# Performance work log

Hardware: AMD Instinct MI355X
Metric: run time of the kernel (lower is better)

The kernel has to match this reference:

```python
import jax, jax.numpy as jnp
import numpy as np

NEG_SLOPE = 0.01  # nn.LeakyReLU default


def gcn_conv(x, src, dst, deg_inv_sqrt, W, b, n_nodes):
    """PyG GCNConv with self-loops already folded into (src, dst, deg_inv_sqrt).
    out = scatter_add(norm_e * (x @ W)[src]) + b, norm_e = d_src^-1/2 * d_dst^-1/2."""
    h = x @ W  # [N, F_out] -- transform first (F_out < F_in saves gather traffic)
    norm = (deg_inv_sqrt[src] * deg_inv_sqrt[dst])[:, None]  # [E, 1]
    msg = h[src] * norm  # [E, F_out]
    return jax.ops.segment_sum(msg, dst, num_segments=n_nodes) + b


def setup_inputs() -> dict:
    key = jax.random.key(0)
    ks = jax.random.split(key, 8)
    N, E, F_IN, F_HID, F_OUT = 50000, 800000, 256, 128, 64
    x = jax.random.normal(ks[0], (N, F_IN), dtype=jnp.float32)
    edge_index = jax.random.randint(ks[1], (2, E), 0, N, dtype=jnp.int64)
    def glorot(k, shape):
        lim = float(np.sqrt(6.0 / (shape[0] + shape[1])))
        return jax.random.uniform(k, shape, jnp.float32, -lim, lim)
    return {
        "x": x,
        "edge_index": edge_index,
        "W1": glorot(ks[2], (F_IN, F_HID)),
        "b1": jnp.zeros((F_HID,), jnp.float32),
        "W_mu": glorot(ks[3], (F_HID, F_OUT)),
        "b_mu": jnp.zeros((F_OUT,), jnp.float32),
        "W_logvar": glorot(ks[4], (F_HID, F_OUT)),
        "b_logvar": jnp.zeros((F_OUT,), jnp.float32),
    }


def reference(x, edge_index, W1, b1, W_mu, b_mu, W_logvar, b_logvar):
    n_nodes = x.shape[0]
    loops = jnp.arange(n_nodes, dtype=edge_index.dtype)
    src = jnp.concatenate([edge_index[0], loops])
    dst = jnp.concatenate([edge_index[1], loops])
    # degree on destination nodes (includes self-loop); >= 1 so rsqrt is safe
    deg = jax.ops.segment_sum(jnp.ones_like(dst, dtype=x.dtype), dst, num_segments=n_nodes)
    deg_inv_sqrt = jax.lax.rsqrt(deg)

    h = gcn_conv(x, src, dst, deg_inv_sqrt, W1, b1, n_nodes)
    h = jax.nn.leaky_relu(h, NEG_SLOPE)
    mu = gcn_conv(h, src, dst, deg_inv_sqrt, W_mu, b_mu, n_nodes)
    logvar = gcn_conv(h, src, dst, deg_inv_sqrt, W_logvar, b_logvar, n_nodes)
    return (mu, logvar)
```

## Files before the change

### kernel.cpp

```cpp
#include <hip/hip_runtime.h>

#define NEG_SLOPE 0.01f
#define EPB 4096
#define NB_SHIFT 8

typedef __attribute__((ext_vector_type(8))) short bf16x8;
typedef __attribute__((ext_vector_type(4))) float floatx4;

__device__ __forceinline__ short f2bf(float f) {
    union { float f; unsigned u; } v; v.f = f;
    unsigned u = v.u;
    u += 0x7FFF + ((u >> 16) & 1);
    return (short)(u >> 16);
}
__device__ __forceinline__ float bf2f(short s) {
    union { unsigned u; float f; } v;
    v.u = ((unsigned)(unsigned short)s) << 16;
    return v.f;
}


__launch_bounds__(256)
__global__ void hist_pack(const int* __restrict__ dst, int E, int B, int K,
                          int* __restrict__ btot,
                          const float* __restrict__ W1, const float* __restrict__ Wmu,
                          const float* __restrict__ Wlv,
                          short* __restrict__ w1f, short* __restrict__ wcatf) {
    __shared__ int lh[256];
    int bid = blockIdx.x;
    if (bid < B) {
        lh[threadIdx.x] = 0;
        __syncthreads();
        int lo = bid * EPB, hi = min(lo + EPB, E);
        for (int e = lo + threadIdx.x; e < hi; e += 256)
            atomicAdd(&lh[dst[e] >> NB_SHIFT], 1);
        __syncthreads();
        int v = lh[threadIdx.x];
        if (v) atomicAdd(&btot[threadIdx.x], v);
    } else {
        int i = (bid - B) * 256 + threadIdx.x;
        if (i < 128 * 256) {
            int j  = i & 7;
            int ln = (i >> 3) & 15;
            int q  = (i >> 7) & 3;
            int t  = (i >> 9) & 7;
            int kb = i >> 12;
            int n = t * 16 + ln;
            int k = kb * 32 + q * 8 + j;
            w1f[i] = f2bf(W1[k * 128 + n]);
        } else {
            int i2 = i - 128 * 256;
            int j  = i2 & 7;
            int ln = (i2 >> 3) & 15;
            int q  = (i2 >> 7) & 3;
            int t  = (i2 >> 9) & 7;
            int kb = i2 >> 12;
            int n = t * 16 + ln;
            int k = kb * 32 + q * 8 + j;
            wcatf[i2] = f2bf((n < 64) ? Wmu[k * 64 + n] : Wlv[k * 64 + (n - 64)]);
        }
    }
}

__global__ void bucket_scan(const int* __restrict__ btot, int K, int E,
                            int* __restrict__ bstart, int* __restrict__ bcur) {
    __shared__ int waveTot[4];
    __shared__ int waveOff[4];
    int tid = threadIdx.x;
    int lane = tid & 63, wave = tid >> 6;
    int v = (tid < K) ? btot[tid] : 0;
    int s = v;
    #pragma unroll
    for (int o = 1; o < 64; o <<= 1) {
        int t = __shfl_up(s, o);
        if (lane >= o) s += t;
    }
    if (lane == 63) waveTot[wave] = s;
    __syncthreads();
    if (tid == 0) {
        int acc = 0;
        #pragma unroll
        for (int w = 0; w < 4; w++) { waveOff[w] = acc; acc += waveTot[w]; }
    }
    __syncthreads();
    int excl = s - v + waveOff[wave];
    if (tid < K) { bstart[tid] = excl; bcur[tid] = excl; }
    if (tid == 0) bstart[K] = E;
}


template<int K, bool ABF16, bool SCALE>
__device__ __forceinline__ void gemm_body(int blk, int tid, const void* __restrict__ Ap,
                                          const short* __restrict__ Bfrag,
                                          short* __restrict__ C, int M,
                                          const float* __restrict__ dis) {
    int w = tid >> 6;
    int lane = tid & 63;
    int ln = lane & 15;
    int q  = lane >> 4;
    int rowTile = blk * 128 + w * 32;

    int r0 = rowTile + ln;
    int r1 = rowTile + 16 + ln;
    int r0c = (r0 < M) ? r0 : (M - 1);
    int r1c = (r1 < M) ? r1 : (M - 1);

    const float* a0F = (const float*)Ap + (size_t)r0c * K + q * 8;
    const float* a1F = (const float*)Ap + (size_t)r1c * K + q * 8;
    const short* a0B = (const short*)Ap + (size_t)r0c * K + q * 8;
    const short* a1B = (const short*)Ap + (size_t)r1c * K + q * 8;
    const short* bLane = Bfrag + lane * 8;

    floatx4 acc[2][8];
    #pragma unroll
    for (int f = 0; f < 2; f++)
        #pragma unroll
        for (int t = 0; t < 8; t++) acc[f][t] = (floatx4){0.f, 0.f, 0.f, 0.f};

    constexpr int NIT = K / 32;
    #pragma unroll
    for (int kb = 0; kb < NIT; kb++) {
        int kt = kb * 32;
        bf16x8 aF0, aF1;
        if (ABF16) {
            aF0 = *(const bf16x8*)(a0B + kt);
            aF1 = *(const bf16x8*)(a1B + kt);
        } else {
            float4 x0 = *(const float4*)(a0F + kt);
            float4 x1 = *(const float4*)(a0F + kt + 4);
            float4 y0 = *(const float4*)(a1F + kt);
            float4 y1 = *(const float4*)(a1F + kt + 4);
            aF0[0] = f2bf(x0.x); aF0[1] = f2bf(x0.y); aF0[2] = f2bf(x0.z); aF0[3] = f2bf(x0.w);
            aF0[4] = f2bf(x1.x); aF0[5] = f2bf(x1.y); aF0[6] = f2bf(x1.z); aF0[7] = f2bf(x1.w);
            aF1[0] = f2bf(y0.x); aF1[1] = f2bf(y0.y); aF1[2] = f2bf(y0.z); aF1[3] = f2bf(y0.w);
            aF1[4] = f2bf(y1.x); aF1[5] = f2bf(y1.y); aF1[6] = f2bf(y1.z); aF1[7] = f2bf(y1.w);
        }
        bf16x8 bF[8];
        #pragma unroll
        for (int t = 0; t < 8; t++)
            bF[t] = *(const bf16x8*)(bLane + (size_t)(kb * 8 + t) * 512);
        #pragma unroll
        for (int t = 0; t < 8; t++) {
            acc[0][t] = __builtin_amdgcn_mfma_f32_16x16x32_bf16(aF0, bF[t], acc[0][t], 0, 0, 0);
            acc[1][t] = __builtin_amdgcn_mfma_f32_16x16x32_bf16(aF1, bF[t], acc[1][t], 0, 0, 0);
        }
    }

    #pragma unroll
    for (int f = 0; f < 2; f++) {
        #pragma unroll
        for (int reg = 0; reg < 4; reg++) {
            int r = rowTile + f * 16 + q * 4 + reg;
            if (r < M) {
                float s = SCALE ? dis[r] : 1.f;
                #pragma unroll
                for (int t = 0; t < 8; t++)
                    C[(size_t)r * 128 + t * 16 + ln] = f2bf(s * acc[f][t][reg]);
            }
        }
    }
}

__launch_bounds__(256)
__global__ void scatter_gemm1(const int* __restrict__ src, const int* __restrict__ dst,
                              int E, int B, int* __restrict__ bcur,
                              unsigned* __restrict__ bucketed,
                              const float* __restrict__ x, const short* __restrict__ w1f,
                              short* __restrict__ z1, int M) {
    __shared__ int lh[256];
    __shared__ int lofs[256];
    __shared__ int gbase[256];
    __shared__ unsigned srt[EPB];
    __shared__ int waveTot[4];
    __shared__ int waveOff[4];
    int bid = blockIdx.x;
    int tid = threadIdx.x;
    if (bid < B) {
        lh[tid] = 0;
        __syncthreads();
        int lo = bid * EPB, hi = min(lo + EPB, E);
        for (int e = lo + tid; e < hi; e += 256)
            atomicAdd(&lh[dst[e] >> NB_SHIFT], 1);
        __syncthreads();
        int v = lh[tid];
        int lane = tid & 63, wave = tid >> 6;
        int s = v;
        #pragma unroll
        for (int o = 1; o < 64; o <<= 1) {
            int t = __shfl_up(s, o);
            if (lane >= o) s += t;
        }
        if (lane == 63) waveTot[wave] = s;
        __syncthreads();
        if (tid == 0) {
            int acc = 0;
            #pragma unroll
            for (int w = 0; w < 4; w++) { waveOff[w] = acc; acc += waveTot[w]; }
        }
        __syncthreads();
        int excl = s - v + waveOff[wave];
        lofs[tid] = excl;
        if (v) gbase[tid] = atomicAdd(&bcur[tid], v);
        __syncthreads();
        lh[tid] = excl;
        __syncthreads();
        for (int e = lo + tid; e < hi; e += 256) {
            int d = dst[e];
            unsigned rec = (unsigned)(src[e] & 0xFFFF) | ((unsigned)d << 16);
            int p = atomicAdd(&lh[d >> NB_SHIFT], 1);
            srt[p] = rec;
        }
        __syncthreads();
        int cnt = hi - lo;
        for (int p = tid; p < cnt; p += 256) {
            unsigned r = srt[p];
            int k = r >> 24;
            bucketed[gbase[k] + (p - lofs[k])] = r;
        }
    } else {
        gemm_body<256, false, false>(bid - B, tid, (const void*)x, w1f, z1, M, nullptr);
    }
}

__global__ void fill_csr_deg(const unsigned* __restrict__ bucketed,
                             const int* __restrict__ bstart,
                             int* __restrict__ row_ptr, int* __restrict__ row_end,
                             float* __restrict__ dis,
                             unsigned short* __restrict__ csr_src, int N) {
    __shared__ int cnt[256];
    __shared__ int rp[256];
    __shared__ int waveTot[4];
    __shared__ int waveOff[4];
    __shared__ unsigned short lcsr[8192];
    int k = blockIdx.x;
    int tid = threadIdx.x;
    int base = k << NB_SHIFT;
    cnt[tid] = 0;
    __syncthreads();
    int lo = bstart[k], hi = bstart[k + 1];
    int m = hi - lo;
    for (int e = lo + tid; e < hi; e += 256)
        atomicAdd(&cnt[(bucketed[e] >> 16) & 255], 1);
    __syncthreads();
    int v = cnt[tid];
    int lane = tid & 63, wave = tid >> 6;
    int s = v;
    #pragma unroll
    for (int o = 1; o < 64; o <<= 1) {
        int t = __shfl_up(s, o);
        if (lane >= o) s += t;
    }
    if (lane == 63) waveTot[wave] = s;
    __syncthreads();
    if (tid == 0) {
        int acc = 0;
        #pragma unroll
        for (int w = 0; w < 4; w++) { waveOff[w] = acc; acc += waveTot[w]; }
    }
    __syncthreads();
    int excl = s - v + waveOff[wave];
    rp[tid] = excl;
    int node = base + tid;
    if (node < N) {
        row_ptr[node] = lo + excl;
        row_end[node] = lo + excl + v;
        dis[node] = rsqrtf(1.0f + (float)v);
    }
    __syncthreads();
    if (m <= 8192) {
        for (int e = lo + tid; e < hi; e += 256) {
            unsigned sd = bucketed[e];
            int p = atomicAdd(&rp[(sd >> 16) & 255], 1);
            lcsr[p] = (unsigned short)(sd & 0xFFFFu);
        }
        __syncthreads();
        for (int i = tid; i < m; i += 256) csr_src[lo + i] = lcsr[i];
    } else {
        for (int e = lo + tid; e < hi; e += 256) {
            unsigned sd = bucketed[e];
            int p = atomicAdd(&rp[(sd >> 16) & 255], 1);
            csr_src[lo + p] = (unsigned short)(sd & 0xFFFFu);
        }
    }
}


__launch_bounds__(256)
__global__ void agg_layer1(const short* __restrict__ z1, const int* __restrict__ row_ptr,
                           const int* __restrict__ row_end,
                           const unsigned short* __restrict__ csr_src,
                           const float* __restrict__ dis, const float* __restrict__ b1,
                           short* __restrict__ h, int N) {
    int wave = threadIdx.x >> 6;
    int node = blockIdx.x * 4 + wave;
    if (node >= N) return;
    int lane = threadIdx.x & 63;
    int qi = lane >> 4;
    int fl = lane & 15;
    int fo = fl * 8;
    const short* zb = z1 + fo;
    int start = row_ptr[node], end = row_end[node];
    float acc[8];
    #pragma unroll
    for (int t = 0; t < 8; t++) acc[t] = 0.f;
    for (int bse = start; bse < end; bse += 64) {
        int n = end - bse; n = (n > 64) ? 64 : n;
        int idx = (int)csr_src[bse + ((lane < n) ? lane : 0)];
        float dl = dis[idx];
        for (int j = 0; j < n; j += 8) {
            int j0 = j + qi;
            int j1 = j0 + 4;
            int c0 = (j0 < n) ? j0 : 0;
            int c1 = (j1 < n) ? j1 : 0;
            int s0 = __shfl(idx, c0);
            int s1 = __shfl(idx, c1);
            float d0 = __shfl(dl, c0);
            float d1 = __shfl(dl, c1);
            if (j0 >= n) d0 = 0.f;
            if (j1 >= n) d1 = 0.f;
            bf16x8 z0 = *(const bf16x8*)(zb + (size_t)s0 * 128);
            bf16x8 zv1 = *(const bf16x8*)(zb + (size_t)s1 * 128);
            #pragma unroll
            for (int t = 0; t < 8; t++)
                acc[t] = fmaf(d0, bf2f(z0[t]), fmaf(d1, bf2f(zv1[t]), acc[t]));
        }
    }
    if (qi == 0) {
        float dn = dis[node];
        bf16x8 zs = *(const bf16x8*)(zb + (size_t)node * 128);
        #pragma unroll
        for (int t = 0; t < 8; t++) acc[t] = fmaf(dn, bf2f(zs[t]), acc[t]);
    }
    #pragma unroll
    for (int t = 0; t < 8; t++) {
        acc[t] += __shfl_xor(acc[t], 16);
        acc[t] += __shfl_xor(acc[t], 32);
    }
    if (qi == 0) {
        float d = dis[node];
        bf16x8 ov;
        #pragma unroll
        for (int t = 0; t < 8; t++) {
            float v = fmaf(d, acc[t], b1[fo + t]);
            v = (v > 0.f) ? v : NEG_SLOPE * v;
            ov[t] = f2bf(v);
        }
        *(bf16x8*)(h + (size_t)node * 128 + fo) = ov;
    }
}


__launch_bounds__(256)
__global__ void agg_layer2(const short* __restrict__ zp, const int* __restrict__ row_ptr,
                           const int* __restrict__ row_end,
                           const unsigned short* __restrict__ csr_src,
                           const float* __restrict__ dis, const float* __restrict__ b_mu,
                           const float* __restrict__ b_lv, float* __restrict__ out, int N) {
    int wave = threadIdx.x >> 6;
    int node = blockIdx.x * 4 + wave;
    if (node >= N) return;
    int lane = threadIdx.x & 63;
    int qi = lane >> 4;
    int fl = lane & 15;
    int fo = fl * 8;
    const short* zb = zp + fo;
    int start = row_ptr[node], end = row_end[node];
    float acc[8];
    #pragma unroll
    for (int t = 0; t < 8; t++) acc[t] = 0.f;
    for (int bse = start; bse < end; bse += 64) {
        int n = end - bse; n = (n > 64) ? 64 : n;
        int idx = (int)csr_src[bse + ((lane < n) ? lane : 0)];
        for (int j = 0; j < n; j += 8) {
            int j0 = j + qi;
            int j1 = j0 + 4;
            int c0 = (j0 < n) ? j0 : 0;
            int c1 = (j1 < n) ? j1 : 0;
            int s0 = __shfl(idx, c0);
            int s1 = __shfl(idx, c1);
            float w0 = (j0 < n) ? 1.f : 0.f;
            float w1 = (j1 < n) ? 1.f : 0.f;
            bf16x8 z0 = *(const bf16x8*)(zb + (size_t)s0 * 128);
            bf16x8 zv1 = *(const bf16x8*)(zb + (size_t)s1 * 128);
            #pragma unroll
            for (int t = 0; t < 8; t++)
                acc[t] = fmaf(w0, bf2f(z0[t]), fmaf(w1, bf2f(zv1[t]), acc[t]));
        }
    }
    if (qi == 0) {
        bf16x8 zs = *(const bf16x8*)(zb + (size_t)node * 128);
        #pragma unroll
        for (int t = 0; t < 8; t++) acc[t] += bf2f(zs[t]);
    }
    #pragma unroll
    for (int t = 0; t < 8; t++) {
        acc[t] += __shfl_xor(acc[t], 16);
        acc[t] += __shfl_xor(acc[t], 32);
    }
    if (qi == 0) {
        float d = dis[node];
        float r[8];
        if (fl < 8) {
            #pragma unroll
            for (int t = 0; t < 8; t++) r[t] = fmaf(d, acc[t], b_mu[fo + t]);
            float* p = out + (size_t)node * 64 + fo;
            *(float4*)p       = make_float4(r[0], r[1], r[2], r[3]);
            *(float4*)(p + 4) = make_float4(r[4], r[5], r[6], r[7]);
        } else {
            #pragma unroll
            for (int t = 0; t < 8; t++) r[t] = fmaf(d, acc[t], b_lv[fo - 64 + t]);
            float* p = out + (size_t)N * 64 + (size_t)node * 64 + (fo - 64);
            *(float4*)p       = make_float4(r[0], r[1], r[2], r[3]);
            *(float4*)(p + 4) = make_float4(r[4], r[5], r[6], r[7]);
        }
    }
}

__launch_bounds__(256)
__global__ void gemm2_kernel(const short* __restrict__ h, const short* __restrict__ wcatf,
                             short* __restrict__ z2, int M, const float* __restrict__ dis) {
    gemm_body<128, true, true>(blockIdx.x, threadIdx.x, (const void*)h, wcatf, z2, M, dis);
}


extern "C" void kernel_launch(void* const* d_in, const int* in_sizes, int n_in,
                              void* d_out, int out_size, void* d_ws, size_t ws_size,
                              hipStream_t stream) {
    const float* x   = (const float*)d_in[0];
    const int*   ei  = (const int*)d_in[1];
    const float* W1  = (const float*)d_in[2];
    const float* b1  = (const float*)d_in[3];
    const float* Wmu = (const float*)d_in[4];
    const float* bmu = (const float*)d_in[5];
    const float* Wlv = (const float*)d_in[6];
    const float* blv = (const float*)d_in[7];
    float* out = (float*)d_out;

    const int F_IN = 256;
    int N = in_sizes[0] / F_IN;
    int E = in_sizes[1] / 2;
    const int* e_src = ei;
    const int* e_dst = ei + E;

    int B = (E + EPB - 1) / EPB;
    int K = (N + 255) >> NB_SHIFT;
    int Ggemm = (N + 127) / 128;

    char* ws = (char*)d_ws;
    size_t off = 0;
    auto carve = [&](size_t bytes) -> void* {
        void* p = ws + off;
        off += (bytes + 255) & ~(size_t)255;
        return p;
    };
    int*      row_end  = (int*)   carve((size_t)N * 4);
    int*      row_ptr  = (int*)   carve((size_t)N * 4);
    float*    dis      = (float*) carve((size_t)N * 4);
    unsigned short* csr_src = (unsigned short*)carve((size_t)E * 2);
    short*    bufA     = (short*) carve((size_t)N * 128 * 2);
    short*    bufB     = (short*) carve((size_t)N * 128 * 2);
    short*    w1f      = (short*) carve(128 * 256 * 2);
    short*    wcatf    = (short*) carve(128 * 128 * 2);
    int*      bstart   = (int*)   carve((size_t)(K + 1) * 4);
    int*      bcur     = (int*)   carve((size_t)K * 4);
    int*      btot     = (int*)   carve((size_t)K * 4);
    unsigned* bucketed = (unsigned*)carve((size_t)E * 4);

    hipMemsetAsync(btot, 0, (size_t)K * 4, stream);
    hipLaunchKernelGGL(hist_pack, dim3(B + 192), dim3(256), 0, stream,
                       e_dst, E, B, K, btot, W1, Wmu, Wlv, w1f, wcatf);
    hipLaunchKernelGGL(bucket_scan, dim3(1), dim3(256), 0, stream, btot, K, E, bstart, bcur);
    hipLaunchKernelGGL(scatter_gemm1, dim3(B + Ggemm), dim3(256), 0, stream,
                       e_src, e_dst, E, B, bcur, bucketed, x, w1f, bufA, N);
    hipLaunchKernelGGL(fill_csr_deg, dim3(K), dim3(256), 0, stream,
                       bucketed, bstart, row_ptr, row_end, dis, csr_src, N);
    hipLaunchKernelGGL(agg_layer1, dim3((N + 3) / 4), dim3(256), 0, stream,
                       bufA, row_ptr, row_end, csr_src, dis, b1, bufB, N);
    hipLaunchKernelGGL(gemm2_kernel, dim3(Ggemm), dim3(256), 0, stream,
                       bufB, wcatf, bufA, N, dis);
    hipLaunchKernelGGL(agg_layer2, dim3((N + 3) / 4), dim3(256), 0, stream,
                       bufA, row_ptr, row_end, csr_src, dis, bmu, blv, out, N);
}
```

Baseline: 222.2 us.

## Slice feature matrices into 32-column planes and aggregate per slice

Intermediate bf16 feature buffers are stored as four column-sliced planes of 32 features ([4][N][32]) instead of row-major [N][128]. The GEMM epilogue and A-operand loads are adapted to this layout. Both aggregation kernels launch four times as many blocks, each handling one slice, so the gathered rows are 64 bytes and each slice's working set (about 3.2MB) fits better in cache. Outputs are written with nontemporal stores. In exchange, CSR indices and degree factors are read four times, and each wave now does a deeper cross-lane reduction.

```diff
diff --git a/kernel.cpp b/kernel.cpp
--- a/kernel.cpp
+++ b/kernel.cpp
@@ -6,6 +6,7 @@
 
 typedef __attribute__((ext_vector_type(8))) short bf16x8;
 typedef __attribute__((ext_vector_type(4))) float floatx4;
+typedef __attribute__((ext_vector_type(4))) unsigned int uintx4;
 
 __device__ __forceinline__ short f2bf(float f) {
     union { float f; unsigned u; } v; v.f = f;
@@ -18,7 +19,14 @@
     v.u = ((unsigned)(unsigned short)s) << 16;
     return v.f;
 }
-
+__device__ __forceinline__ void nt_store16(void* p, bf16x8 v) {
+    union { bf16x8 b; uintx4 u; } cv; cv.b = v;
+    __builtin_nontemporal_store(cv.u, (uintx4*)p);
+}
+__device__ __forceinline__ void nt_store_f4(float* p, float a, float b, float c, float d) {
+    floatx4 v = (floatx4){a, b, c, d};
+    __builtin_nontemporal_store(v, (floatx4*)p);
+}
 
 __launch_bounds__(256)
 __global__ void hist_pack(const int* __restrict__ dst, int E, int B, int K,
@@ -89,7 +97,7 @@
 }
 
 
-template<int K, bool ABF16, bool SCALE>
+template<int K, bool ASLICED, bool SCALE>
 __device__ __forceinline__ void gemm_body(int blk, int tid, const void* __restrict__ Ap,
                                           const short* __restrict__ Bfrag,
                                           short* __restrict__ C, int M,
@@ -107,8 +115,8 @@
 
     const float* a0F = (const float*)Ap + (size_t)r0c * K + q * 8;
     const float* a1F = (const float*)Ap + (size_t)r1c * K + q * 8;
-    const short* a0B = (const short*)Ap + (size_t)r0c * K + q * 8;
-    const short* a1B = (const short*)Ap + (size_t)r1c * K + q * 8;
+    const short* a0B = (const short*)Ap + (size_t)r0c * 32 + q * 8;
+    const short* a1B = (const short*)Ap + (size_t)r1c * 32 + q * 8;
     const short* bLane = Bfrag + lane * 8;
 
     floatx4 acc[2][8];
@@ -120,12 +128,12 @@
     constexpr int NIT = K / 32;
     #pragma unroll
     for (int kb = 0; kb < NIT; kb++) {
-        int kt = kb * 32;
         bf16x8 aF0, aF1;
-        if (ABF16) {
-            aF0 = *(const bf16x8*)(a0B + kt);
-            aF1 = *(const bf16x8*)(a1B + kt);
+        if (ASLICED) {
+            aF0 = *(const bf16x8*)(a0B + (size_t)kb * M * 32);
+            aF1 = *(const bf16x8*)(a1B + (size_t)kb * M * 32);
         } else {
+            int kt = kb * 32;
             float4 x0 = *(const float4*)(a0F + kt);
             float4 x1 = *(const float4*)(a0F + kt + 4);
             float4 y0 = *(const float4*)(a1F + kt);
@@ -152,10 +160,11 @@
         for (int reg = 0; reg < 4; reg++) {
             int r = rowTile + f * 16 + q * 4 + reg;
             if (r < M) {
-                float s = SCALE ? dis[r] : 1.f;
+                float sc = SCALE ? dis[r] : 1.f;
                 #pragma unroll
                 for (int t = 0; t < 8; t++)
-                    C[(size_t)r * 128 + t * 16 + ln] = f2bf(s * acc[f][t][reg]);
+                    C[((size_t)(t >> 1) * M + r) * 32 + (t & 1) * 16 + ln] =
+                        f2bf(sc * acc[f][t][reg]);
             }
         }
     }
@@ -290,15 +299,17 @@
                            const int* __restrict__ row_end,
                            const unsigned short* __restrict__ csr_src,
                            const float* __restrict__ dis, const float* __restrict__ b1,
-                           short* __restrict__ h, int N) {
+                           short* __restrict__ h, int N, int NB) {
     int wave = threadIdx.x >> 6;
-    int node = blockIdx.x * 4 + wave;
+    int s  = blockIdx.x / NB;
+    int nb = blockIdx.x - s * NB;
+    int node = nb * 4 + wave;
     if (node >= N) return;
     int lane = threadIdx.x & 63;
-    int qi = lane >> 4;
-    int fl = lane & 15;
+    int g  = lane >> 2;
+    int fl = lane & 3;
     int fo = fl * 8;
-    const short* zb = z1 + fo;
+    const short* zb = z1 + (size_t)s * N * 32 + fo;
     int start = row_ptr[node], end = row_end[node];
     float acc[8];
     #pragma unroll
@@ -307,9 +318,9 @@
         int n = end - bse; n = (n > 64) ? 64 : n;
         int idx = (int)csr_src[bse + ((lane < n) ? lane : 0)];
         float dl = dis[idx];
-        for (int j = 0; j < n; j += 8) {
-            int j0 = j + qi;
-            int j1 = j0 + 4;
+        for (int j = 0; j < n; j += 32) {
+            int j0 = j + g;
+            int j1 = j0 + 16;
             int c0 = (j0 < n) ? j0 : 0;
             int c1 = (j1 < n) ? j1 : 0;
             int s0 = __shfl(idx, c0);
@@ -318,52 +329,56 @@
             float d1 = __shfl(dl, c1);
             if (j0 >= n) d0 = 0.f;
             if (j1 >= n) d1 = 0.f;
-            bf16x8 z0 = *(const bf16x8*)(zb + (size_t)s0 * 128);
-            bf16x8 zv1 = *(const bf16x8*)(zb + (size_t)s1 * 128);
+            bf16x8 z0 = *(const bf16x8*)(zb + (size_t)s0 * 32);
+            bf16x8 zv = *(const bf16x8*)(zb + (size_t)s1 * 32);
             #pragma unroll
             for (int t = 0; t < 8; t++)
-                acc[t] = fmaf(d0, bf2f(z0[t]), fmaf(d1, bf2f(zv1[t]), acc[t]));
-        }
-    }
-    if (qi == 0) {
+                acc[t] = fmaf(d0, bf2f(z0[t]), fmaf(d1, bf2f(zv[t]), acc[t]));
+        }
+    }
+    if (g == 0) {
         float dn = dis[node];
-        bf16x8 zs = *(const bf16x8*)(zb + (size_t)node * 128);
+        bf16x8 zs = *(const bf16x8*)(zb + (size_t)node * 32);
         #pragma unroll
         for (int t = 0; t < 8; t++) acc[t] = fmaf(dn, bf2f(zs[t]), acc[t]);
     }
     #pragma unroll
     for (int t = 0; t < 8; t++) {
+        acc[t] += __shfl_xor(acc[t], 4);
+        acc[t] += __shfl_xor(acc[t], 8);
         acc[t] += __shfl_xor(acc[t], 16);
         acc[t] += __shfl_xor(acc[t], 32);
     }
-    if (qi == 0) {
+    if (g == 0) {
         float d = dis[node];
         bf16x8 ov;
         #pragma unroll
         for (int t = 0; t < 8; t++) {
-            float v = fmaf(d, acc[t], b1[fo + t]);
+            float v = fmaf(d, acc[t], b1[s * 32 + fo + t]);
             v = (v > 0.f) ? v : NEG_SLOPE * v;
             ov[t] = f2bf(v);
         }
-        *(bf16x8*)(h + (size_t)node * 128 + fo) = ov;
-    }
-}
-
+        nt_store16(h + (size_t)s * N * 32 + (size_t)node * 32 + fo, ov);
+    }
+}
 
 __launch_bounds__(256)
 __global__ void agg_layer2(const short* __restrict__ zp, const int* __restrict__ row_ptr,
                            const int* __restrict__ row_end,
                            const unsigned short* __restrict__ csr_src,
                            const float* __restrict__ dis, const float* __restrict__ b_mu,
-                           const float* __restrict__ b_lv, float* __restrict__ out, int N) {
+                           const float* __restrict__ b_lv, float* __restrict__ out,
+                           int N, int NB) {
     int wave = threadIdx.x >> 6;
-    int node = blockIdx.x * 4 + wave;
+    int s  = blockIdx.x / NB;
+    int nb = blockIdx.x - s * NB;
+    int node = nb * 4 + wave;
     if (node >= N) return;
     int lane = threadIdx.x & 63;
-    int qi = lane >> 4;
-    int fl = lane & 15;
+    int g  = lane >> 2;
+    int fl = lane & 3;
     int fo = fl * 8;
-    const short* zb = zp + fo;
+    const short* zb = zp + (size_t)s * N * 32 + fo;
     int start = row_ptr[node], end = row_end[node];
     float acc[8];
     #pragma unroll
@@ -371,47 +386,49 @@
     for (int bse = start; bse < end; bse += 64) {
         int n = end - bse; n = (n > 64) ? 64 : n;
         int idx = (int)csr_src[bse + ((lane < n) ? lane : 0)];
-        for (int j = 0; j < n; j += 8) {
-            int j0 = j + qi;
-            int j1 = j0 + 4;
+        for (int j = 0; j < n; j += 32) {
+            int j0 = j + g;
+            int j1 = j0 + 16;
             int c0 = (j0 < n) ? j0 : 0;
             int c1 = (j1 < n) ? j1 : 0;
             int s0 = __shfl(idx, c0);
             int s1 = __shfl(idx, c1);
             float w0 = (j0 < n) ? 1.f : 0.f;
             float w1 = (j1 < n) ? 1.f : 0.f;
-            bf16x8 z0 = *(const bf16x8*)(zb + (size_t)s0 * 128);
-            bf16x8 zv1 = *(const bf16x8*)(zb + (size_t)s1 * 128);
+            bf16x8 z0 = *(const bf16x8*)(zb + (size_t)s0 * 32);
+            bf16x8 zv = *(const bf16x8*)(zb + (size_t)s1 * 32);
             #pragma unroll
             for (int t = 0; t < 8; t++)
-                acc[t] = fmaf(w0, bf2f(z0[t]), fmaf(w1, bf2f(zv1[t]), acc[t]));
-        }
-    }
-    if (qi == 0) {
-        bf16x8 zs = *(const bf16x8*)(zb + (size_t)node * 128);
+                acc[t] = fmaf(w0, bf2f(z0[t]), fmaf(w1, bf2f(zv[t]), acc[t]));
+        }
+    }
+    if (g == 0) {
+        bf16x8 zs = *(const bf16x8*)(zb + (size_t)node * 32);
         #pragma unroll
         for (int t = 0; t < 8; t++) acc[t] += bf2f(zs[t]);
     }
     #pragma unroll
     for (int t = 0; t < 8; t++) {
+        acc[t] += __shfl_xor(acc[t], 4);
+        acc[t] += __shfl_xor(acc[t], 8);
         acc[t] += __shfl_xor(acc[t], 16);
         acc[t] += __shfl_xor(acc[t], 32);
     }
-    if (qi == 0) {
+    if (g == 0) {
         float d = dis[node];
         float r[8];
-        if (fl < 8) {
+        if (s < 2) {
             #pragma unroll
-            for (int t = 0; t < 8; t++) r[t] = fmaf(d, acc[t], b_mu[fo + t]);
-            float* p = out + (size_t)node * 64 + fo;
-            *(float4*)p       = make_float4(r[0], r[1], r[2], r[3]);
-            *(float4*)(p + 4) = make_float4(r[4], r[5], r[6], r[7]);
+            for (int t = 0; t < 8; t++) r[t] = fmaf(d, acc[t], b_mu[s * 32 + fo + t]);
+            float* p = out + (size_t)node * 64 + s * 32 + fo;
+            nt_store_f4(p,     r[0], r[1], r[2], r[3]);
+            nt_store_f4(p + 4, r[4], r[5], r[6], r[7]);
         } else {
             #pragma unroll
-            for (int t = 0; t < 8; t++) r[t] = fmaf(d, acc[t], b_lv[fo - 64 + t]);
-            float* p = out + (size_t)N * 64 + (size_t)node * 64 + (fo - 64);
-            *(float4*)p       = make_float4(r[0], r[1], r[2], r[3]);
-            *(float4*)(p + 4) = make_float4(r[4], r[5], r[6], r[7]);
+            for (int t = 0; t < 8; t++) r[t] = fmaf(d, acc[t], b_lv[(s - 2) * 32 + fo + t]);
+            float* p = out + (size_t)N * 64 + (size_t)node * 64 + (s - 2) * 32 + fo;
+            nt_store_f4(p,     r[0], r[1], r[2], r[3]);
+            nt_store_f4(p + 4, r[4], r[5], r[6], r[7]);
         }
     }
 }
@@ -445,6 +462,7 @@
     int B = (E + EPB - 1) / EPB;
     int K = (N + 255) >> NB_SHIFT;
     int Ggemm = (N + 127) / 128;
+    int NB = (N + 3) / 4;
 
     char* ws = (char*)d_ws;
     size_t off = 0;
@@ -474,10 +492,10 @@
                        e_src, e_dst, E, B, bcur, bucketed, x, w1f, bufA, N);
     hipLaunchKernelGGL(fill_csr_deg, dim3(K), dim3(256), 0, stream,
                        bucketed, bstart, row_ptr, row_end, dis, csr_src, N);
-    hipLaunchKernelGGL(agg_layer1, dim3((N + 3) / 4), dim3(256), 0, stream,
-                       bufA, row_ptr, row_end, csr_src, dis, b1, bufB, N);
+    hipLaunchKernelGGL(agg_layer1, dim3(4 * NB), dim3(256), 0, stream,
+                       bufA, row_ptr, row_end, csr_src, dis, b1, bufB, N, NB);
     hipLaunchKernelGGL(gemm2_kernel, dim3(Ggemm), dim3(256), 0, stream,
                        bufB, wcatf, bufA, N, dis);
-    hipLaunchKernelGGL(agg_layer2, dim3((N + 3) / 4), dim3(256), 0, stream,
-                       bufA, row_ptr, row_end, csr_src, dis, bmu, blv, out, N);
-}
+    hipLaunchKernelGGL(agg_layer2, dim3(4 * NB), dim3(256), 0, stream,
+                       bufA, row_ptr, row_end, csr_src, dis, bmu, blv, out, N, NB);
+}
```

Result: slower. 323.1 us (+45.4%).

## Fuse layer-1 aggregation with second GEMM via LDS tile

Applied to the files above, without the earlier changes.

Merges the layer-1 neighbor aggregation and the mu/logvar GEMM into one kernel. Each block aggregates 64 nodes into a swizzled LDS tile, then runs MFMA on that tile against the concatenated weights. This drops the round trip of the hidden activations through global memory and one kernel launch. In exchange each wave now processes 16 nodes serially, so there are fewer blocks in flight and less latency hiding for the irregular gathers.

```diff
diff --git a/kernel.cpp b/kernel.cpp
--- a/kernel.cpp
+++ b/kernel.cpp
@@ -28,17 +28,18 @@
                           short* __restrict__ w1f, short* __restrict__ wcatf) {
     __shared__ int lh[256];
     int bid = blockIdx.x;
+    int tid = threadIdx.x;
     if (bid < B) {
-        lh[threadIdx.x] = 0;
+        lh[tid] = 0;
         __syncthreads();
         int lo = bid * EPB, hi = min(lo + EPB, E);
-        for (int e = lo + threadIdx.x; e < hi; e += 256)
+        for (int e = lo + tid; e < hi; e += 256)
             atomicAdd(&lh[dst[e] >> NB_SHIFT], 1);
         __syncthreads();
-        int v = lh[threadIdx.x];
-        if (v) atomicAdd(&btot[threadIdx.x], v);
+        int v = lh[tid];
+        if (v) atomicAdd(&btot[tid], v);
     } else {
-        int i = (bid - B) * 256 + threadIdx.x;
+        int i = (bid - B) * 256 + tid;
         if (i < 128 * 256) {
             int j  = i & 7;
             int ln = (i >> 3) & 15;
@@ -88,12 +89,10 @@
     if (tid == 0) bstart[K] = E;
 }
 
-
-template<int K, bool ABF16, bool SCALE>
-__device__ __forceinline__ void gemm_body(int blk, int tid, const void* __restrict__ Ap,
-                                          const short* __restrict__ Bfrag,
-                                          short* __restrict__ C, int M,
-                                          const float* __restrict__ dis) {
+template<int K>
+__device__ __forceinline__ void gemm1_body(int blk, int tid, const float* __restrict__ Ap,
+                                           const short* __restrict__ Bfrag,
+                                           short* __restrict__ C, int M) {
     int w = tid >> 6;
     int lane = tid & 63;
     int ln = lane & 15;
@@ -105,10 +104,8 @@
     int r0c = (r0 < M) ? r0 : (M - 1);
     int r1c = (r1 < M) ? r1 : (M - 1);
 
-    const float* a0F = (const float*)Ap + (size_t)r0c * K + q * 8;
-    const float* a1F = (const float*)Ap + (size_t)r1c * K + q * 8;
-    const short* a0B = (const short*)Ap + (size_t)r0c * K + q * 8;
-    const short* a1B = (const short*)Ap + (size_t)r1c * K + q * 8;
+    const float* a0F = Ap + (size_t)r0c * K + q * 8;
+    const float* a1F = Ap + (size_t)r1c * K + q * 8;
     const short* bLane = Bfrag + lane * 8;
 
     floatx4 acc[2][8];
@@ -122,19 +119,14 @@
     for (int kb = 0; kb < NIT; kb++) {
         int kt = kb * 32;
         bf16x8 aF0, aF1;
-        if (ABF16) {
-            aF0 = *(const bf16x8*)(a0B + kt);
-            aF1 = *(const bf16x8*)(a1B + kt);
-        } else {
-            float4 x0 = *(const float4*)(a0F + kt);
-            float4 x1 = *(const float4*)(a0F + kt + 4);
-            float4 y0 = *(const float4*)(a1F + kt);
-            float4 y1 = *(const float4*)(a1F + kt + 4);
-            aF0[0] = f2bf(x0.x); aF0[1] = f2bf(x0.y); aF0[2] = f2bf(x0.z); aF0[3] = f2bf(x0.w);
-            aF0[4] = f2bf(x1.x); aF0[5] = f2bf(x1.y); aF0[6] = f2bf(x1.z); aF0[7] = f2bf(x1.w);
-            aF1[0] = f2bf(y0.x); aF1[1] = f2bf(y0.y); aF1[2] = f2bf(y0.z); aF1[3] = f2bf(y0.w);
-            aF1[4] = f2bf(y1.x); aF1[5] = f2bf(y1.y); aF1[6] = f2bf(y1.z); aF1[7] = f2bf(y1.w);
-        }
+        float4 x0 = *(const float4*)(a0F + kt);
+        float4 x1 = *(const float4*)(a0F + kt + 4);
+        float4 y0 = *(const float4*)(a1F + kt);
+        float4 y1 = *(const float4*)(a1F + kt + 4);
+        aF0[0] = f2bf(x0.x); aF0[1] = f2bf(x0.y); aF0[2] = f2bf(x0.z); aF0[3] = f2bf(x0.w);
+        aF0[4] = f2bf(x1.x); aF0[5] = f2bf(x1.y); aF0[6] = f2bf(x1.z); aF0[7] = f2bf(x1.w);
+        aF1[0] = f2bf(y0.x); aF1[1] = f2bf(y0.y); aF1[2] = f2bf(y0.z); aF1[3] = f2bf(y0.w);
+        aF1[4] = f2bf(y1.x); aF1[5] = f2bf(y1.y); aF1[6] = f2bf(y1.z); aF1[7] = f2bf(y1.w);
         bf16x8 bF[8];
         #pragma unroll
         for (int t = 0; t < 8; t++)
@@ -152,10 +144,9 @@
         for (int reg = 0; reg < 4; reg++) {
             int r = rowTile + f * 16 + q * 4 + reg;
             if (r < M) {
-                float s = SCALE ? dis[r] : 1.f;
                 #pragma unroll
                 for (int t = 0; t < 8; t++)
-                    C[(size_t)r * 128 + t * 16 + ln] = f2bf(s * acc[f][t][reg]);
+                    C[(size_t)r * 128 + t * 16 + ln] = f2bf(acc[f][t][reg]);
             }
         }
     }
@@ -218,7 +209,7 @@
             bucketed[gbase[k] + (p - lofs[k])] = r;
         }
     } else {
-        gemm_body<256, false, false>(bid - B, tid, (const void*)x, w1f, z1, M, nullptr);
+        gemm1_body<256>(bid - B, tid, x, w1f, z1, M);
     }
 }
 
@@ -286,69 +277,126 @@
 
 
 __launch_bounds__(256)
-__global__ void agg_layer1(const short* __restrict__ z1, const int* __restrict__ row_ptr,
+__global__ void agg1_gemm2(const short* __restrict__ z1, const int* __restrict__ row_ptr,
                            const int* __restrict__ row_end,
                            const unsigned short* __restrict__ csr_src,
                            const float* __restrict__ dis, const float* __restrict__ b1,
-                           short* __restrict__ h, int N) {
-    int wave = threadIdx.x >> 6;
-    int node = blockIdx.x * 4 + wave;
-    if (node >= N) return;
-    int lane = threadIdx.x & 63;
+                           const short* __restrict__ wcatf,
+                           short* __restrict__ z2, int N) {
+    __shared__ short htile[64 * 128];
+    int tid = threadIdx.x;
+    int w = tid >> 6;
+    int lane = tid & 63;
     int qi = lane >> 4;
     int fl = lane & 15;
     int fo = fl * 8;
+    int base = blockIdx.x * 64;
+
     const short* zb = z1 + fo;
-    int start = row_ptr[node], end = row_end[node];
-    float acc[8];
-    #pragma unroll
-    for (int t = 0; t < 8; t++) acc[t] = 0.f;
-    for (int bse = start; bse < end; bse += 64) {
-        int n = end - bse; n = (n > 64) ? 64 : n;
-        int idx = (int)csr_src[bse + ((lane < n) ? lane : 0)];
-        float dl = dis[idx];
-        for (int j = 0; j < n; j += 8) {
-            int j0 = j + qi;
-            int j1 = j0 + 4;
-            int c0 = (j0 < n) ? j0 : 0;
-            int c1 = (j1 < n) ? j1 : 0;
-            int s0 = __shfl(idx, c0);
-            int s1 = __shfl(idx, c1);
-            float d0 = __shfl(dl, c0);
-            float d1 = __shfl(dl, c1);
-            if (j0 >= n) d0 = 0.f;
-            if (j1 >= n) d1 = 0.f;
-            bf16x8 z0 = *(const bf16x8*)(zb + (size_t)s0 * 128);
-            bf16x8 zv1 = *(const bf16x8*)(zb + (size_t)s1 * 128);
+    for (int i = 0; i < 16; ++i) {
+        int local = w * 16 + i;
+        int node = base + local;
+        int swz = ((local & 7) * 8);
+        short* hrow = &htile[(local * 128 + fo) ^ swz];
+        if (node < N) {
+            int start = row_ptr[node], end = row_end[node];
+            float acc[8];
             #pragma unroll
-            for (int t = 0; t < 8; t++)
-                acc[t] = fmaf(d0, bf2f(z0[t]), fmaf(d1, bf2f(zv1[t]), acc[t]));
-        }
-    }
-    if (qi == 0) {
-        float dn = dis[node];
-        bf16x8 zs = *(const bf16x8*)(zb + (size_t)node * 128);
-        #pragma unroll
-        for (int t = 0; t < 8; t++) acc[t] = fmaf(dn, bf2f(zs[t]), acc[t]);
-    }
-    #pragma unroll
-    for (int t = 0; t < 8; t++) {
-        acc[t] += __shfl_xor(acc[t], 16);
-        acc[t] += __shfl_xor(acc[t], 32);
-    }
-    if (qi == 0) {
-        float d = dis[node];
-        bf16x8 ov;
-        #pragma unroll
-        for (int t = 0; t < 8; t++) {
-            float v = fmaf(d, acc[t], b1[fo + t]);
-            v = (v > 0.f) ? v : NEG_SLOPE * v;
-            ov[t] = f2bf(v);
-        }
-        *(bf16x8*)(h + (size_t)node * 128 + fo) = ov;
-    }
-}
-
+            for (int t = 0; t < 8; t++) acc[t] = 0.f;
+            for (int bse = start; bse < end; bse += 64) {
+                int n = end - bse; n = (n > 64) ? 64 : n;
+                int idx = (int)csr_src[bse + ((lane < n) ? lane : 0)];
+                float dl = dis[idx];
+                for (int j = 0; j < n; j += 8) {
+                    int j0 = j + qi;
+                    int j1 = j0 + 4;
+                    int c0 = (j0 < n) ? j0 : 0;
+                    int c1 = (j1 < n) ? j1 : 0;
+                    int s0 = __shfl(idx, c0);
+                    int s1 = __shfl(idx, c1);
+                    float d0 = __shfl(dl, c0);
+                    float d1 = __shfl(dl, c1);
+                    if (j0 >= n) d0 = 0.f;
+                    if (j1 >= n) d1 = 0.f;
+                    bf16x8 zv0 = *(const bf16x8*)(zb + (size_t)s0 * 128);
+                    bf16x8 zv1 = *(const bf16x8*)(zb + (size_t)s1 * 128);
+                    #pragma unroll
+                    for (int t = 0; t < 8; t++)
+                        acc[t] = fmaf(d0, bf2f(zv0[t]), fmaf(d1, bf2f(zv1[t]), acc[t]));
+                }
+            }
+            if (qi == 0) {
+                float dn = dis[node];
+                bf16x8 zs = *(const bf16x8*)(zb + (size_t)node * 128);
+                #pragma unroll
+                for (int t = 0; t < 8; t++) acc[t] = fmaf(dn, bf2f(zs[t]), acc[t]);
+            }
+            #pragma unroll
+            for (int t = 0; t < 8; t++) {
+                acc[t] += __shfl_xor(acc[t], 16);
+                acc[t] += __shfl_xor(acc[t], 32);
+            }
+            if (qi == 0) {
+                float d = dis[node];
+                bf16x8 ov;
+                #pragma unroll
+                for (int t = 0; t < 8; t++) {
+                    float v = fmaf(d, acc[t], b1[fo + t]);
+                    v = (v > 0.f) ? v : NEG_SLOPE * v;
+                    ov[t] = f2bf(v);
+                }
+                *(bf16x8*)hrow = ov;
+            }
+        } else if (qi == 0) {
+            *(bf16x8*)hrow = (bf16x8){0, 0, 0, 0, 0, 0, 0, 0};
+        }
+    }
+    __syncthreads();
+
+    int rw = (w & 1) * 32;
+    int tc = (w >> 1) * 4;
+    int ln = fl;
+    int q  = qi;
+    int r0 = rw + ln;
+    int r1 = rw + 16 + ln;
+    const short* bLane = wcatf + lane * 8;
+
+    floatx4 acc[2][4];
+    #pragma unroll
+    for (int f = 0; f < 2; f++)
+        #pragma unroll
+        for (int t = 0; t < 4; t++) acc[f][t] = (floatx4){0.f, 0.f, 0.f, 0.f};
+
+    #pragma unroll
+    for (int kb = 0; kb < 4; kb++) {
+        int k0 = kb * 32 + q * 8;
+        bf16x8 aF0 = *(const bf16x8*)&htile[(r0 * 128 + k0) ^ ((r0 & 7) * 8)];
+        bf16x8 aF1 = *(const bf16x8*)&htile[(r1 * 128 + k0) ^ ((r1 & 7) * 8)];
+        bf16x8 bF[4];
+        #pragma unroll
+        for (int t = 0; t < 4; t++)
+            bF[t] = *(const bf16x8*)(bLane + (size_t)(kb * 8 + tc + t) * 512);
+        #pragma unroll
+        for (int t = 0; t < 4; t++) {
+            acc[0][t] = __builtin_amdgcn_mfma_f32_16x16x32_bf16(aF0, bF[t], acc[0][t], 0, 0, 0);
+            acc[1][t] = __builtin_amdgcn_mfma_f32_16x16x32_bf16(aF1, bF[t], acc[1][t], 0, 0, 0);
+        }
+    }
+
+    #pragma unroll
+    for (int f = 0; f < 2; f++) {
+        #pragma unroll
+        for (int reg = 0; reg < 4; reg++) {
+            int gr = base + rw + f * 16 + q * 4 + reg;
+            if (gr < N) {
+                float s = dis[gr];
+                #pragma unroll
+                for (int t = 0; t < 4; t++)
+                    z2[(size_t)gr * 128 + (tc + t) * 16 + ln] = f2bf(s * acc[f][t][reg]);
+            }
+        }
+    }
+}
 
 __launch_bounds__(256)
 __global__ void agg_layer2(const short* __restrict__ zp, const int* __restrict__ row_ptr,
@@ -416,12 +464,6 @@
     }
 }
 
-__launch_bounds__(256)
-__global__ void gemm2_kernel(const short* __restrict__ h, const short* __restrict__ wcatf,
-                             short* __restrict__ z2, int M, const float* __restrict__ dis) {
-    gemm_body<128, true, true>(blockIdx.x, threadIdx.x, (const void*)h, wcatf, z2, M, dis);
-}
-
 
 extern "C" void kernel_launch(void* const* d_in, const int* in_sizes, int n_in,
                               void* d_out, int out_size, void* d_ws, size_t ws_size,
@@ -445,6 +487,7 @@
     int B = (E + EPB - 1) / EPB;
     int K = (N + 255) >> NB_SHIFT;
     int Ggemm = (N + 127) / 128;
+    int G2 = (N + 63) / 64;
 
     char* ws = (char*)d_ws;
     size_t off = 0;
@@ -474,10 +517,8 @@
                        e_src, e_dst, E, B, bcur, bucketed, x, w1f, bufA, N);
     hipLaunchKernelGGL(fill_csr_deg, dim3(K), dim3(256), 0, stream,
                        bucketed, bstart, row_ptr, row_end, dis, csr_src, N);
-    hipLaunchKernelGGL(agg_layer1, dim3((N + 3) / 4), dim3(256), 0, stream,
-                       bufA, row_ptr, row_end, csr_src, dis, b1, bufB, N);
-    hipLaunchKernelGGL(gemm2_kernel, dim3(Ggemm), dim3(256), 0, stream,
-                       bufB, wcatf, bufA, N, dis);
+    hipLaunchKernelGGL(agg1_gemm2, dim3(G2), dim3(256), 0, stream,
+                       bufA, row_ptr, row_end, csr_src, dis, b1, wcatf, bufB, N);
     hipLaunchKernelGGL(agg_layer2, dim3((N + 3) / 4), dim3(256), 0, stream,
-                       bufA, row_ptr, row_end, csr_src, dis, bmu, blv, out, N);
-}
+                       bufB, row_ptr, row_end, csr_src, dis, bmu, blv, out, N);
+}
```

Result: slower. 232.1 us (+4.4%).
